# Performance work log

Hardware: AMD Instinct MI355X
Metric: run time of the kernel (lower is better)

The kernel has to match this reference:

```python
import jax, jax.numpy as jnp
import numpy as np

INPUT_SZ = 256
HIDDEN_SZ = 256


def setup_inputs() -> dict:
    key = jax.random.key(0)
    ks = jax.random.split(key, 14)
    stdv = 1.0 / np.sqrt(HIDDEN_SZ)
    def u(k, shape):
        return jax.random.uniform(k, shape, jnp.float32, -stdv, stdv)
    x = jax.random.normal(ks[0], (32, 2048, INPUT_SZ), jnp.float32)
    return {
        'x': x,
        'W_f': u(ks[1], (INPUT_SZ, HIDDEN_SZ)), 'U_f': u(ks[2], (HIDDEN_SZ, HIDDEN_SZ)), 'b_f': u(ks[3], (HIDDEN_SZ,)),
        'W_i': u(ks[4], (INPUT_SZ, HIDDEN_SZ)), 'U_i': u(ks[5], (HIDDEN_SZ, HIDDEN_SZ)), 'b_i': u(ks[6], (HIDDEN_SZ,)),
        'W_o': u(ks[7], (INPUT_SZ, HIDDEN_SZ)), 'U_o': u(ks[8], (HIDDEN_SZ, HIDDEN_SZ)), 'b_o': u(ks[9], (HIDDEN_SZ,)),
        'W_c': u(ks[10], (INPUT_SZ, HIDDEN_SZ)), 'U_c': u(ks[11], (HIDDEN_SZ, HIDDEN_SZ)), 'b_c': u(ks[12], (HIDDEN_SZ,)),
    }


def _lstm(x, W_f, U_f, b_f, W_i, U_i, b_i, W_o, U_o, b_o, W_c, U_c, b_c):
    B, S, _ = x.shape
    H = b_f.shape[0]
    # Fuse the 4 input-projection GEMMs into one big matmul over all timesteps.
    W = jnp.concatenate([W_f, W_i, W_c, W_o], axis=1)  # [I, 4H]
    U = jnp.concatenate([U_f, U_i, U_c, U_o], axis=1)  # [H, 4H]
    b = jnp.concatenate([b_f, b_i, b_c, b_o])          # [4H]
    xg = jnp.einsum('bsi,ig->bsg', x, W) + b           # [B, S, 4H]
    h0 = jnp.zeros((B, H), x.dtype)
    c0 = jnp.zeros((B, H), x.dtype)

    def step(carry, xg_t):
        h, c = carry
        z = xg_t + h @ U                                # [B, 4H]
        f = jax.nn.sigmoid(z[:, 0 * H:1 * H])
        i = jax.nn.sigmoid(z[:, 1 * H:2 * H])
        g = jnp.tanh(z[:, 2 * H:3 * H])
        o = jax.nn.sigmoid(z[:, 3 * H:4 * H])
        c = f * c + i * g
        h = o * jnp.tanh(c)
        return (h, c), h

    (h_t, c_t), hidden_seq = jax.lax.scan(step, (h0, c0), jnp.swapaxes(xg, 0, 1))
    hidden_seq = jnp.swapaxes(hidden_seq, 0, 1)         # [B, S, H]
    return hidden_seq, (h_t, c_t)


def reference(x, W_f, U_f, b_f, W_i, U_i, b_i, W_o, U_o, b_o, W_c, U_c, b_c):
    return _lstm(x, W_f, U_f, b_f, W_i, U_i, b_i, W_o, U_o, b_o, W_c, U_c, b_c)
```

## Files before the change

### kernel.cpp

```cpp
#include <hip/hip_runtime.h>


typedef int    v4i  __attribute__((ext_vector_type(4)));
typedef float  v4f  __attribute__((ext_vector_type(4)));
typedef __bf16 v8bf __attribute__((ext_vector_type(8)));

#define LOG2E 1.442695040888963f

__device__ __forceinline__ float fast_sigmoid(float x) {
    return __builtin_amdgcn_rcpf(1.f + __builtin_amdgcn_exp2f(-LOG2E * x));
}
__device__ __forceinline__ float fast_tanh(float x) {
    return 1.f - 2.f * __builtin_amdgcn_rcpf(__builtin_amdgcn_exp2f(2.f * LOG2E * x) + 1.f);
}

__device__ __forceinline__ void async_copy16(const void* g, void* l) {
    __builtin_amdgcn_global_load_lds(
        (const __attribute__((address_space(1))) unsigned int*)g,
        (__attribute__((address_space(3))) unsigned int*)l, 16, 0, 0);
}

__global__ void prep_kernel(
    const float* __restrict__ Wf, const float* __restrict__ Wi,
    const float* __restrict__ Wc, const float* __restrict__ Wo,
    const float* __restrict__ Uf, const float* __restrict__ Ui,
    const float* __restrict__ Uc, const float* __restrict__ Uo,
    __bf16* __restrict__ WT, signed char* __restrict__ qUT,
    float* __restrict__ scales)
{
    int n = blockIdx.x;
    int lane = threadIdx.x;
    if (n < 1024) {
        const float* src = (n < 256) ? Wf : (n < 512) ? Wi : (n < 768) ? Wc : Wo;
        int c = n & 255;
        #pragma unroll
        for (int q = 0; q < 4; ++q) {
            int k = q * 64 + lane;
            WT[n * 256 + k] = (__bf16)src[k * 256 + c];
        }
    } else {
        int nn = n - 1024;
        const float* src = (nn < 256) ? Uf : (nn < 512) ? Ui : (nn < 768) ? Uc : Uo;
        int c = nn & 255;
        float v[4];
        float m = 0.f;
        #pragma unroll
        for (int q = 0; q < 4; ++q) {
            v[q] = src[(q * 64 + lane) * 256 + c];
            m = fmaxf(m, fabsf(v[q]));
        }
        #pragma unroll
        for (int s = 1; s < 64; s <<= 1) m = fmaxf(m, __shfl_xor(m, s));
        float inv = (m > 1e-20f) ? (127.f / m) : 0.f;
        #pragma unroll
        for (int q = 0; q < 4; ++q) {
            int qq = (int)__builtin_rintf(v[q] * inv);
            qUT[nn * 256 + q * 64 + lane] = (signed char)qq;
        }
        if (lane == 0) scales[nn] = m / 16129.f;
    }
}

__global__ __launch_bounds__(256) void proj_kernel(
    const float* __restrict__ x, const __bf16* __restrict__ WT,
    const float* __restrict__ bf_, const float* __restrict__ bi_,
    const float* __restrict__ bc_, const float* __restrict__ bo_,
    __bf16* __restrict__ xg, int t0)
{
    int tid = threadIdx.x;
    int lane = tid & 63, wid = tid >> 6;
    int quad = lane >> 4, l16 = lane & 15;
    int bx = blockIdx.x;
    int by = blockIdx.y;

    int lr = by * 64 + wid * 16 + l16;
    int r = t0 * 32 + lr;
    int bb = r & 31, tt = r >> 5;
    const float* xrow = x + (bb * 2048 + tt) * 256;

    v4f acc[8] = {};
    #pragma unroll
    for (int kt = 0; kt < 8; ++kt) {
        int k = kt * 32 + quad * 8;
        v4f a0 = *(const v4f*)(xrow + k);
        v4f a1 = *(const v4f*)(xrow + k + 4);
        v8bf af;
        #pragma unroll
        for (int j = 0; j < 4; ++j) { af[j] = (__bf16)a0[j]; af[4 + j] = (__bf16)a1[j]; }
        #pragma unroll
        for (int nt = 0; nt < 8; ++nt) {
            int n = bx * 128 + nt * 16 + l16;
            v8bf bfr = *(const v8bf*)(WT + n * 256 + k);
            acc[nt] = __builtin_amdgcn_mfma_f32_16x16x32_bf16(af, bfr, acc[nt], 0, 0, 0);
        }
    }
    #pragma unroll
    for (int nt = 0; nt < 8; ++nt) {
        int n = bx * 128 + nt * 16 + l16;
        const float* bsrc = (n < 256) ? bf_ : (n < 512) ? bi_ : (n < 768) ? bc_ : bo_;
        float bias = bsrc[n & 255];
        #pragma unroll
        for (int rg = 0; rg < 4; ++rg) {
            int lrow = by * 64 + wid * 16 + quad * 4 + rg;
            xg[lrow * 1024 + n] = (__bf16)(acc[nt][rg] + bias);
        }
    }
}

#define SLOT 8320
#define QHB  1152

__global__ __launch_bounds__(512, 2) void lstm_rec_kernel(
    const __bf16* __restrict__ xg,
    const signed char* __restrict__ qUT,
    const float* __restrict__ scales,
    float* __restrict__ out,
    int t0, int Tc,
    signed char* __restrict__ qcarry,
    float* __restrict__ ccarry)
{
    __shared__ __align__(16) char ring[4 * SLOT];
    __shared__ __align__(16) signed char qh[2 * QHB];

    const int tid = threadIdx.x;
    const int lane = tid & 63, wid = tid >> 6;
    const int quad = lane >> 4, l16 = lane & 15;
    const int b0 = blockIdx.x * 4;
    const bool arow = (l16 & 3) == 0;
    const int bq = l16 >> 2;

    v4i bfr[8][4];
    float scl[8];
    int jcol[8];
    #pragma unroll
    for (int g = 0; g < 4; ++g) {
        #pragma unroll
        for (int jh = 0; jh < 2; ++jh) {
            int tl = g * 2 + jh;
            int n = g * 256 + wid * 32 + jh * 16 + l16;
            jcol[tl] = n;
            scl[tl] = scales[n];
            #pragma unroll
            for (int kt = 0; kt < 4; ++kt)
                bfr[tl][kt] = *(const v4i*)(qUT + n * 256 + kt * 64 + quad * 16);
        }
    }

    for (int i = tid; i < (2 * QHB) / 4; i += 512) ((int*)qh)[i] = 0;
    __syncthreads();

    float c0 = 0.f, c1 = 0.f;
    const int j0 = wid * 32 + l16;
    if (t0 != 0) {
        qh[quad * 288 + j0]      = qcarry[(b0 + quad) * 256 + j0];
        qh[quad * 288 + j0 + 16] = qcarry[(b0 + quad) * 256 + j0 + 16];
        c0 = ccarry[(b0 + quad) * 256 + j0];
        c1 = ccarry[(b0 + quad) * 256 + j0 + 16];
    }

    const char* xgb = (const char*)xg;
    const int wrow = wid >> 1, whalf = wid & 1;
    #pragma unroll
    for (int s = 0; s < 3; ++s) {
        if (s < Tc) {
            long src = ((long)(s * 32 + b0 + wrow)) * 2048 + whalf * 1024 + (long)lane * 16;
            char* dst = ring + s * SLOT + wrow * 2080 + whalf * 1024;
            async_copy16(xgb + src, dst);
        }
    }

    float* orow = out + ((long)(b0 + quad)) * 2048 * 256 + j0;
    float hreg[4][2];

    for (int tl4 = 0; tl4 < Tc; tl4 += 4) {
        #pragma unroll
        for (int u = 0; u < 4; ++u) {
            const int tl = tl4 + u;
            const int t = t0 + tl;

            __syncthreads();

            if (tl + 3 < Tc) {
                long src = ((long)((tl + 3) * 32 + b0 + wrow)) * 2048 + whalf * 1024 + (long)lane * 16;
                char* dst = ring + ((u + 3) & 3) * SLOT + wrow * 2080 + whalf * 1024;
                async_copy16(xgb + src, dst);
            }

            const signed char* qA = qh + (u & 1) * QHB;
            signed char* qB = qh + ((u + 1) & 1) * QHB;
            const char* xb = ring + (u & 3) * SLOT + quad * 2080;

            v4i a[4];
            #pragma unroll
            for (int kt = 0; kt < 4; ++kt) {
                v4i z = (v4i){0, 0, 0, 0};
                a[kt] = arow ? *(const v4i*)(qA + bq * 288 + kt * 64 + quad * 16) : z;
            }
            float xv[8];
            #pragma unroll
            for (int g = 0; g < 8; ++g)
                xv[g] = (float)(*(const __bf16*)(xb + jcol[g] * 2));

            v4i acc[8];
            #pragma unroll
            for (int g = 0; g < 8; ++g) acc[g] = (v4i){0, 0, 0, 0};
            #pragma unroll
            for (int kt = 0; kt < 4; ++kt) {
                #pragma unroll
                for (int g = 0; g < 8; ++g)
                    acc[g] = __builtin_amdgcn_mfma_i32_16x16x64_i8(a[kt], bfr[g][kt], acc[g], 0, 0, 0);
            }

            #pragma unroll
            for (int jh = 0; jh < 2; ++jh) {
                float zf = xv[0 + jh] + scl[0 + jh] * (float)acc[0 + jh][0];
                float zi = xv[2 + jh] + scl[2 + jh] * (float)acc[2 + jh][0];
                float zg = xv[4 + jh] + scl[4 + jh] * (float)acc[4 + jh][0];
                float zo = xv[6 + jh] + scl[6 + jh] * (float)acc[6 + jh][0];
                float f  = fast_sigmoid(zf);
                float i_ = fast_sigmoid(zi);
                float g_ = fast_tanh(zg);
                float o_ = fast_sigmoid(zo);
                float c = (jh == 0) ? c0 : c1;
                c = f * c + i_ * g_;
                if (jh == 0) c0 = c; else c1 = c;
                float h = o_ * fast_tanh(c);
                hreg[u][jh] = h;

                int j = j0 + jh * 16;
                int q = (int)__builtin_rintf(h * 127.f);
                qB[quad * 288 + j] = (signed char)q;
                if (t == 2047) {
                    out[16777216 + (b0 + quad) * 256 + j] = h;
                    out[16785408 + (b0 + quad) * 256 + j] = c;
                }
                if (tl == Tc - 1) {
                    qcarry[(b0 + quad) * 256 + j] = (signed char)q;
                    ccarry[(b0 + quad) * 256 + j] = c;
                }
            }

            if (u == 3) {
                #pragma unroll
                for (int s = 0; s < 4; ++s) {
                    long ts = t - 3 + s;
                    orow[ts * 256]      = hreg[s][0];
                    orow[ts * 256 + 16] = hreg[s][1];
                }
            }
        }
    }
}

extern "C" void kernel_launch(void* const* d_in, const int* in_sizes, int n_in,
                              void* d_out, int out_size, void* d_ws, size_t ws_size,
                              hipStream_t stream) {
    const float* x   = (const float*)d_in[0];
    const float* Wf  = (const float*)d_in[1];
    const float* Uf  = (const float*)d_in[2];
    const float* bf_ = (const float*)d_in[3];
    const float* Wi  = (const float*)d_in[4];
    const float* Ui  = (const float*)d_in[5];
    const float* bi_ = (const float*)d_in[6];
    const float* Wo  = (const float*)d_in[7];
    const float* Uo  = (const float*)d_in[8];
    const float* bo_ = (const float*)d_in[9];
    const float* Wc  = (const float*)d_in[10];
    const float* Uc  = (const float*)d_in[11];
    const float* bc_ = (const float*)d_in[12];

    char* ws = (char*)d_ws;
    __bf16*      WT     = (__bf16*)ws;
    signed char* qUT    = (signed char*)(ws + 524288);
    float*       scales = (float*)(ws + 786432);
    signed char* qcarry = (signed char*)(ws + 790528);
    float*       ccarry = (float*)(ws + 798720);
    __bf16*      xg     = (__bf16*)(ws + 831488);

    size_t avail = (ws_size > 831488) ? ws_size - 831488 : 0;
    int Tc = 2048;
    while (Tc > 8 && (size_t)Tc * 65536ULL > avail) Tc >>= 1;

    prep_kernel<<<dim3(2048), dim3(64), 0, stream>>>(
        Wf, Wi, Wc, Wo, Uf, Ui, Uc, Uo, WT, qUT, scales);
    for (int t0 = 0; t0 < 2048; t0 += Tc) {
        proj_kernel<<<dim3(8, Tc / 2), dim3(256), 0, stream>>>(
            x, WT, bf_, bi_, bc_, bo_, xg, t0);
        lstm_rec_kernel<<<dim3(8), dim3(512), 0, stream>>>(
            xg, qUT, scales, (float*)d_out, t0, Tc, qcarry, ccarry);
    }
}
```

Baseline: 2.352 ms.

## Double recurrent kernel threads, interleave gate layout, stage projection input in LDS

The recurrent kernel moves from 512 to 1024 threads, so each thread owns one hidden unit instead of two, halving the MFMA and activation work per wave on the serial critical path. The projection kernel now writes xg with the four gates interleaved per hidden unit, so the recurrent kernel reads one 8-byte vector instead of several scattered bf16 loads. The projection kernel also converts each x tile to bf16 once in LDS and loops over all 1024 output columns in one block, which removes the redundant x reads across the former eight column blocks. The cost is fewer projection blocks with a longer serial loop over W, and higher register pressure and barrier cost with 1024-thread blocks in the recurrence.

```diff
diff --git a/kernel.cpp b/kernel.cpp
--- a/kernel.cpp
+++ b/kernel.cpp
@@ -4,6 +4,7 @@
 typedef int    v4i  __attribute__((ext_vector_type(4)));
 typedef float  v4f  __attribute__((ext_vector_type(4)));
 typedef __bf16 v8bf __attribute__((ext_vector_type(8)));
+typedef __bf16 v4bf __attribute__((ext_vector_type(4)));
 
 #define LOG2E 1.442695040888963f
 
@@ -67,42 +68,58 @@
     const float* __restrict__ bc_, const float* __restrict__ bo_,
     __bf16* __restrict__ xg, int t0)
 {
+    __shared__ __align__(16) __bf16 xs[64][264];
+
     int tid = threadIdx.x;
     int lane = tid & 63, wid = tid >> 6;
     int quad = lane >> 4, l16 = lane & 15;
-    int bx = blockIdx.x;
-    int by = blockIdx.y;
-
-    int lr = by * 64 + wid * 16 + l16;
-    int r = t0 * 32 + lr;
-    int bb = r & 31, tt = r >> 5;
-    const float* xrow = x + (bb * 2048 + tt) * 256;
-
-    v4f acc[8] = {};
+    int by = blockIdx.x;
+
+    {
+        int row = tid >> 2, seg = (tid & 3) * 64;
+        int r = t0 * 32 + by * 64 + row;
+        int bb = r & 31, tt = r >> 5;
+        const float* xrow = x + ((long)(bb * 2048 + tt)) * 256 + seg;
+        #pragma unroll
+        for (int q = 0; q < 16; ++q) {
+            v4f v = *(const v4f*)(xrow + q * 4);
+            v4bf o;
+            #pragma unroll
+            for (int j = 0; j < 4; ++j) o[j] = (__bf16)v[j];
+            *(v4bf*)(&xs[row][seg + q * 4]) = o;
+        }
+    }
+    __syncthreads();
+
+    v8bf af[8];
     #pragma unroll
-    for (int kt = 0; kt < 8; ++kt) {
-        int k = kt * 32 + quad * 8;
-        v4f a0 = *(const v4f*)(xrow + k);
-        v4f a1 = *(const v4f*)(xrow + k + 4);
-        v8bf af;
-        #pragma unroll
-        for (int j = 0; j < 4; ++j) { af[j] = (__bf16)a0[j]; af[4 + j] = (__bf16)a1[j]; }
+    for (int kt = 0; kt < 8; ++kt)
+        af[kt] = *(const v8bf*)(&xs[wid * 16 + l16][kt * 32 + quad * 8]);
+
+    #pragma unroll
+    for (int p = 0; p < 8; ++p) {
+        v4f acc[8] = {};
+        #pragma unroll
+        for (int kt = 0; kt < 8; ++kt) {
+            int k = kt * 32 + quad * 8;
+            #pragma unroll
+            for (int nt = 0; nt < 8; ++nt) {
+                int n = p * 128 + nt * 16 + l16;
+                v8bf bfr = *(const v8bf*)(WT + n * 256 + k);
+                acc[nt] = __builtin_amdgcn_mfma_f32_16x16x32_bf16(af[kt], bfr, acc[nt], 0, 0, 0);
+            }
+        }
         #pragma unroll
         for (int nt = 0; nt < 8; ++nt) {
-            int n = bx * 128 + nt * 16 + l16;
-            v8bf bfr = *(const v8bf*)(WT + n * 256 + k);
-            acc[nt] = __builtin_amdgcn_mfma_f32_16x16x32_bf16(af, bfr, acc[nt], 0, 0, 0);
-        }
-    }
-    #pragma unroll
-    for (int nt = 0; nt < 8; ++nt) {
-        int n = bx * 128 + nt * 16 + l16;
-        const float* bsrc = (n < 256) ? bf_ : (n < 512) ? bi_ : (n < 768) ? bc_ : bo_;
-        float bias = bsrc[n & 255];
-        #pragma unroll
-        for (int rg = 0; rg < 4; ++rg) {
-            int lrow = by * 64 + wid * 16 + quad * 4 + rg;
-            xg[lrow * 1024 + n] = (__bf16)(acc[nt][rg] + bias);
+            int n = p * 128 + nt * 16 + l16;
+            const float* bsrc = (n < 256) ? bf_ : (n < 512) ? bi_ : (n < 768) ? bc_ : bo_;
+            float bias = bsrc[n & 255];
+            int colp = (n & 255) * 4 + (n >> 8);
+            #pragma unroll
+            for (int rg = 0; rg < 4; ++rg) {
+                int lrow = by * 64 + wid * 16 + quad * 4 + rg;
+                xg[(long)lrow * 1024 + colp] = (__bf16)(acc[nt][rg] + bias);
+            }
         }
     }
 }
@@ -110,7 +127,7 @@
 #define SLOT 8320
 #define QHB  1152
 
-__global__ __launch_bounds__(512, 2) void lstm_rec_kernel(
+__global__ __launch_bounds__(1024) void lstm_rec_kernel(
     const __bf16* __restrict__ xg,
     const signed char* __restrict__ qUT,
     const float* __restrict__ scales,
@@ -126,51 +143,43 @@
     const int lane = tid & 63, wid = tid >> 6;
     const int quad = lane >> 4, l16 = lane & 15;
     const int b0 = blockIdx.x * 4;
-    const bool arow = (l16 & 3) == 0;
-    const int bq = l16 >> 2;
-
-    v4i bfr[8][4];
-    float scl[8];
-    int jcol[8];
+    const int j = wid * 16 + l16;
+
+    v4i bfr[4][4];
+    float scl[4];
     #pragma unroll
     for (int g = 0; g < 4; ++g) {
-        #pragma unroll
-        for (int jh = 0; jh < 2; ++jh) {
-            int tl = g * 2 + jh;
-            int n = g * 256 + wid * 32 + jh * 16 + l16;
-            jcol[tl] = n;
-            scl[tl] = scales[n];
-            #pragma unroll
-            for (int kt = 0; kt < 4; ++kt)
-                bfr[tl][kt] = *(const v4i*)(qUT + n * 256 + kt * 64 + quad * 16);
-        }
-    }
-
-    for (int i = tid; i < (2 * QHB) / 4; i += 512) ((int*)qh)[i] = 0;
+        int n = g * 256 + j;
+        scl[g] = scales[n];
+        #pragma unroll
+        for (int kt = 0; kt < 4; ++kt)
+            bfr[g][kt] = *(const v4i*)(qUT + n * 256 + kt * 64 + quad * 16);
+    }
+
+    if (tid < (2 * QHB) / 4) ((int*)qh)[tid] = 0;
     __syncthreads();
 
-    float c0 = 0.f, c1 = 0.f;
-    const int j0 = wid * 32 + l16;
+    float c = 0.f;
     if (t0 != 0) {
-        qh[quad * 288 + j0]      = qcarry[(b0 + quad) * 256 + j0];
-        qh[quad * 288 + j0 + 16] = qcarry[(b0 + quad) * 256 + j0 + 16];
-        c0 = ccarry[(b0 + quad) * 256 + j0];
-        c1 = ccarry[(b0 + quad) * 256 + j0 + 16];
+        qh[quad * 288 + j] = qcarry[(b0 + quad) * 256 + j];
+        c = ccarry[(b0 + quad) * 256 + j];
     }
 
     const char* xgb = (const char*)xg;
     const int wrow = wid >> 1, whalf = wid & 1;
-    #pragma unroll
-    for (int s = 0; s < 3; ++s) {
-        if (s < Tc) {
-            long src = ((long)(s * 32 + b0 + wrow)) * 2048 + whalf * 1024 + (long)lane * 16;
-            char* dst = ring + s * SLOT + wrow * 2080 + whalf * 1024;
-            async_copy16(xgb + src, dst);
-        }
-    }
-
-    float* orow = out + ((long)(b0 + quad)) * 2048 * 256 + j0;
-    float hreg[4][2];
+    if (tid < 512) {
+        #pragma unroll
+        for (int s = 0; s < 3; ++s) {
+            if (s < Tc) {
+                long src = ((long)(s * 32 + b0 + wrow)) * 2048 + whalf * 1024 + (long)lane * 16;
+                char* dst = ring + s * SLOT + wrow * 2080 + whalf * 1024;
+                async_copy16(xgb + src, dst);
+            }
+        }
+    }
+
+    float* orow = out + ((long)(b0 + quad)) * 2048 * 256 + j;
+    float hreg[4];
 
     for (int tl4 = 0; tl4 < Tc; tl4 += 4) {
         #pragma unroll
@@ -180,7 +189,7 @@
 
             __syncthreads();
 
-            if (tl + 3 < Tc) {
+            if (tid < 512 && tl + 3 < Tc) {
                 long src = ((long)((tl + 3) * 32 + b0 + wrow)) * 2048 + whalf * 1024 + (long)lane * 16;
                 char* dst = ring + ((u + 3) & 3) * SLOT + wrow * 2080 + whalf * 1024;
                 async_copy16(xgb + src, dst);
@@ -192,62 +201,50 @@
 
             v4i a[4];
             #pragma unroll
-            for (int kt = 0; kt < 4; ++kt) {
-                v4i z = (v4i){0, 0, 0, 0};
-                a[kt] = arow ? *(const v4i*)(qA + bq * 288 + kt * 64 + quad * 16) : z;
-            }
-            float xv[8];
-            #pragma unroll
-            for (int g = 0; g < 8; ++g)
-                xv[g] = (float)(*(const __bf16*)(xb + jcol[g] * 2));
-
-            v4i acc[8];
-            #pragma unroll
-            for (int g = 0; g < 8; ++g) acc[g] = (v4i){0, 0, 0, 0};
+            for (int kt = 0; kt < 4; ++kt)
+                a[kt] = *(const v4i*)(qA + (l16 >> 2) * 288 + kt * 64 + quad * 16);
+
+            v4bf xp = *(const v4bf*)(xb + j * 8);
+
+            v4i acc[4];
+            #pragma unroll
+            for (int g = 0; g < 4; ++g) acc[g] = (v4i){0, 0, 0, 0};
             #pragma unroll
             for (int kt = 0; kt < 4; ++kt) {
                 #pragma unroll
-                for (int g = 0; g < 8; ++g)
+                for (int g = 0; g < 4; ++g)
                     acc[g] = __builtin_amdgcn_mfma_i32_16x16x64_i8(a[kt], bfr[g][kt], acc[g], 0, 0, 0);
             }
 
-            #pragma unroll
-            for (int jh = 0; jh < 2; ++jh) {
-                float zf = xv[0 + jh] + scl[0 + jh] * (float)acc[0 + jh][0];
-                float zi = xv[2 + jh] + scl[2 + jh] * (float)acc[2 + jh][0];
-                float zg = xv[4 + jh] + scl[4 + jh] * (float)acc[4 + jh][0];
-                float zo = xv[6 + jh] + scl[6 + jh] * (float)acc[6 + jh][0];
-                float f  = fast_sigmoid(zf);
-                float i_ = fast_sigmoid(zi);
-                float g_ = fast_tanh(zg);
-                float o_ = fast_sigmoid(zo);
-                float c = (jh == 0) ? c0 : c1;
-                c = f * c + i_ * g_;
-                if (jh == 0) c0 = c; else c1 = c;
-                float h = o_ * fast_tanh(c);
-                hreg[u][jh] = h;
-
-                int j = j0 + jh * 16;
-                int q = (int)__builtin_rintf(h * 127.f);
-                qB[quad * 288 + j] = (signed char)q;
-                if (t == 2047) {
-                    out[16777216 + (b0 + quad) * 256 + j] = h;
-                    out[16785408 + (b0 + quad) * 256 + j] = c;
-                }
-                if (tl == Tc - 1) {
-                    qcarry[(b0 + quad) * 256 + j] = (signed char)q;
-                    ccarry[(b0 + quad) * 256 + j] = c;
-                }
-            }
-
-            if (u == 3) {
-                #pragma unroll
-                for (int s = 0; s < 4; ++s) {
-                    long ts = t - 3 + s;
-                    orow[ts * 256]      = hreg[s][0];
-                    orow[ts * 256 + 16] = hreg[s][1];
-                }
-            }
+            float zf = (float)xp[0] + scl[0] * (float)acc[0][0];
+            float zi = (float)xp[1] + scl[1] * (float)acc[1][0];
+            float zg = (float)xp[2] + scl[2] * (float)acc[2][0];
+            float zo = (float)xp[3] + scl[3] * (float)acc[3][0];
+            float f  = fast_sigmoid(zf);
+            float i_ = fast_sigmoid(zi);
+            float g_ = fast_tanh(zg);
+            float o_ = fast_sigmoid(zo);
+            c = f * c + i_ * g_;
+            float h = o_ * fast_tanh(c);
+            hreg[u] = h;
+
+            int q = (int)__builtin_rintf(h * 127.f);
+            qB[quad * 288 + j] = (signed char)q;
+            if (t == 2047) {
+                out[16777216 + (b0 + quad) * 256 + j] = h;
+                out[16785408 + (b0 + quad) * 256 + j] = c;
+            }
+            if (tl == Tc - 1) {
+                qcarry[(b0 + quad) * 256 + j] = (signed char)q;
+                ccarry[(b0 + quad) * 256 + j] = c;
+            }
+        }
+
+        {
+            long tb = (long)(t0 + tl4) * 256;
+            #pragma unroll
+            for (int s = 0; s < 4; ++s)
+                orow[tb + s * 256] = hreg[s];
         }
     }
 }
@@ -284,9 +281,9 @@
     prep_kernel<<<dim3(2048), dim3(64), 0, stream>>>(
         Wf, Wi, Wc, Wo, Uf, Ui, Uc, Uo, WT, qUT, scales);
     for (int t0 = 0; t0 < 2048; t0 += Tc) {
-        proj_kernel<<<dim3(8, Tc / 2), dim3(256), 0, stream>>>(
+        proj_kernel<<<dim3(Tc / 2), dim3(256), 0, stream>>>(
             x, WT, bf_, bi_, bc_, bo_, xg, t0);
-        lstm_rec_kernel<<<dim3(8), dim3(512), 0, stream>>>(
+        lstm_rec_kernel<<<dim3(8), dim3(1024), 0, stream>>>(
             xg, qUT, scales, (float*)d_out, t0, Tc, qcarry, ccarry);
     }
 }
```

Measured after the change: 1.999 ms. 1.18x faster.
